# Optimization experiments

Hardware: AMD Instinct MI355X
Metric: run time of the kernel (lower is better)

## Reference

```python
import jax, jax.numpy as jnp
import numpy as np

LOSS_WEIGHT = 1.0
INTENSITY_WEIGHT = 0.5


def setup_inputs() -> dict:
    key = jax.random.key(0)
    k1, k2 = jax.random.split(key)
    N = 8192
    adv_pc = jax.random.normal(k1, (N, 4), dtype=jnp.float32)
    ori_pc = jax.random.normal(k2, (N, 4), dtype=jnp.float32)
    return {"adv_pc": adv_pc, "ori_pc": ori_pc}


def reference(adv_pc, ori_pc):
    # Scale the intensity channel (index 3) by intensity_weight, as in forward().
    scale = jnp.array([1.0, 1.0, 1.0, INTENSITY_WEIGHT], dtype=adv_pc.dtype)
    a = adv_pc * scale  # [N, 4]
    b = ori_pc * scale  # [M, 4]
    # knn_points with K=1 returns SQUARED euclidean distance to nearest neighbor.
    # Use the ||a||^2 + ||b||^2 - 2 a.b expansion to avoid an [N, M, 4] diff tensor.
    a2 = jnp.sum(a * a, axis=-1)          # [N]
    b2 = jnp.sum(b * b, axis=-1)          # [M]
    cross = jnp.einsum('nd,md->nm', a, b)  # [N, M]
    sqdist = a2[:, None] + b2[None, :] - 2.0 * cross  # [N, M]
    min_d = jnp.min(sqdist, axis=-1)      # per-adv-point nearest sq distance, [N]
    hd = jnp.max(min_d)                   # one-sided Hausdorff (squared)
    # original keeps the batch dim of size 1 after max(-1)
    return jnp.reshape(hd * LOSS_WEIGHT, (1,))
```

## Files before the change

kernel.cpp:

```cpp
#include <hip/hip_runtime.h>
#include <math.h>

#define THREADS 256
#define APT 4
#define TILE 64
#define RTHREADS 1024

__global__ __launch_bounds__(THREADS) void hd_min_atomic(
    const float* __restrict__ adv, const float* __restrict__ ori,
    int* __restrict__ mins,
    int N, int M, int chunks)
{
    __shared__ float4 sb[TILE];
    __shared__ __align__(16) float sb2[TILE];

    const int tid = threadIdx.x;
    const int base_i = blockIdx.x * (THREADS * APT) + tid;

    float4 a[APT];
    #pragma unroll
    for (int k = 0; k < APT; ++k) {
        int i = base_i + k * THREADS;
        float4 v = make_float4(0.f, 0.f, 0.f, 0.f);
        if (i < N) v = ((const float4*)adv)[i];
        a[k].x = -2.0f * v.x;
        a[k].y = -2.0f * v.y;
        a[k].z = -2.0f * v.z;
        a[k].w = -v.w;
    }

    float m[APT];
    #pragma unroll
    for (int k = 0; k < APT; ++k) m[k] = INFINITY;

    for (int base = blockIdx.y * TILE; base < M; base += chunks * TILE) {
        for (int k = tid; k < TILE; k += THREADS) {
            int j = base + k;
            float4 b = make_float4(0.f, 0.f, 0.f, 0.f);
            float b2 = INFINITY;
            if (j < M) {
                b = ((const float4*)ori)[j];
                b.w *= 0.5f;
                b2 = b.x*b.x + b.y*b.y + b.z*b.z + b.w*b.w;
            }
            sb[k]  = b;
            sb2[k] = b2;
        }
        __syncthreads();

        #pragma unroll 4
        for (int j = 0; j < TILE; j += 4) {
            float4 p0 = sb[j+0], p1 = sb[j+1], p2 = sb[j+2], p3 = sb[j+3];
            float4 q  = ((const float4*)sb2)[j >> 2];
            #pragma unroll
            for (int k = 0; k < APT; ++k) {
                float ax = a[k].x, ay = a[k].y, az = a[k].z, aw = a[k].w;
                float d0 = fmaf(ax, p0.x, fmaf(ay, p0.y, fmaf(az, p0.z, fmaf(aw, p0.w, q.x))));
                float d1 = fmaf(ax, p1.x, fmaf(ay, p1.y, fmaf(az, p1.z, fmaf(aw, p1.w, q.y))));
                float d2 = fmaf(ax, p2.x, fmaf(ay, p2.y, fmaf(az, p2.z, fmaf(aw, p2.w, q.z))));
                float d3 = fmaf(ax, p3.x, fmaf(ay, p3.y, fmaf(az, p3.z, fmaf(aw, p3.w, q.w))));
                m[k] = fminf(m[k], fminf(fminf(d0, d1), fminf(d2, d3)));
            }
        }
        __syncthreads();
    }

    #pragma unroll
    for (int k = 0; k < APT; ++k) {
        int i = base_i + k * THREADS;
        if (i < N) {
            float aa = a[k].x*a[k].x + a[k].y*a[k].y + a[k].z*a[k].z + a[k].w*a[k].w;
            float d  = fmaxf(fmaf(0.25f, aa, m[k]), 0.0f);
            atomicMin(&mins[i], __float_as_int(d));
        }
    }
}

__global__ __launch_bounds__(RTHREADS) void hd_final_max(
    const int* __restrict__ mins, float* __restrict__ out, int N)
{
    float m = 0.0f;
    for (int i = threadIdx.x; i < N; i += RTHREADS)
        m = fmaxf(m, __int_as_float(mins[i]));
    for (int off = 32; off >= 1; off >>= 1)
        m = fmaxf(m, __shfl_down(m, off, 64));
    __shared__ float smax[RTHREADS / 64];
    int lane = threadIdx.x & 63, wave = threadIdx.x >> 6;
    if (lane == 0) smax[wave] = m;
    __syncthreads();
    if (threadIdx.x == 0) {
        float bm = smax[0];
        #pragma unroll
        for (int w = 1; w < RTHREADS / 64; ++w) bm = fmaxf(bm, smax[w]);
        out[0] = bm;
    }
}

extern "C" void kernel_launch(void* const* d_in, const int* in_sizes, int n_in,
                              void* d_out, int out_size, void* d_ws, size_t ws_size,
                              hipStream_t stream) {
    const float* adv = (const float*)d_in[0];
    const float* ori = (const float*)d_in[1];
    float* out = (float*)d_out;
    int*   mins = (int*)d_ws;

    int N = in_sizes[0] / 4;
    int M = in_sizes[1] / 4;

    int gx    = (N + THREADS * APT - 1) / (THREADS * APT);
    int N_pad = gx * THREADS * APT;

    int maxtiles = (M + TILE - 1) / TILE;
    int chunks = 512 / gx;
    if (chunks < 1) chunks = 1;
    if (chunks > maxtiles) chunks = maxtiles;

    hipMemsetAsync(mins, 0x7F, (size_t)N_pad * sizeof(int), stream);

    hd_min_atomic<<<dim3(gx, chunks), THREADS, 0, stream>>>(
        adv, ori, mins, N, M, chunks);
    hd_final_max<<<1, RTHREADS, 0, stream>>>(mins, out, N);
}
```

Baseline: 68.10 us.

## Fuse nearest-neighbor min and Hausdorff max into one packed-FMA kernel

Replaces the memset, the atomicMin kernel and the final max kernel with a single kernel. Each block holds 16 adv points in registers as packed 2-wide vectors and streams all ori points straight from global memory. It reduces each point's minimum with wave shuffles and shared memory, then issues one atomicMax per block into the output. This removes two launches and the per-point workspace traffic, and the packed float2 FMAs aim to double ALU throughput. The trade-off is that every block re-reads the whole ori array (mostly from cache). The output is never zeroed before the atomicMax, so correctness depends on the initial contents of the output buffer.

```diff
diff --git a/kernel.cpp b/kernel.cpp
--- a/kernel.cpp
+++ b/kernel.cpp
@@ -2,97 +2,129 @@
 #include <math.h>
 
 #define THREADS 256
-#define APT 4
-#define TILE 64
-#define RTHREADS 1024
+#define APB 16
 
-__global__ __launch_bounds__(THREADS) void hd_min_atomic(
+typedef float v2f __attribute__((ext_vector_type(2)));
+
+__global__ __launch_bounds__(THREADS) void hd_onepass(
     const float* __restrict__ adv, const float* __restrict__ ori,
-    int* __restrict__ mins,
-    int N, int M, int chunks)
+    float* __restrict__ out, int N, int M)
 {
-    __shared__ float4 sb[TILE];
-    __shared__ __align__(16) float sb2[TILE];
+    __shared__ __align__(16) float4 sadv[APB];
+    __shared__ float sred[4][APB];
 
-    const int tid = threadIdx.x;
-    const int base_i = blockIdx.x * (THREADS * APT) + tid;
+    const int tid  = threadIdx.x;
+    const int base = blockIdx.x * APB;
 
-    float4 a[APT];
-    #pragma unroll
-    for (int k = 0; k < APT; ++k) {
-        int i = base_i + k * THREADS;
+    if (tid < APB) {
+        int i = base + tid;
         float4 v = make_float4(0.f, 0.f, 0.f, 0.f);
         if (i < N) v = ((const float4*)adv)[i];
-        a[k].x = -2.0f * v.x;
-        a[k].y = -2.0f * v.y;
-        a[k].z = -2.0f * v.z;
-        a[k].w = -v.w;
+        sadv[tid] = make_float4(-2.0f*v.x, -2.0f*v.y, -2.0f*v.z, -v.w);
+    }
+    __syncthreads();
+
+    v2f ax[APB/2], ay[APB/2], az[APB/2], aw[APB/2];
+    #pragma unroll
+    for (int p = 0; p < APB/2; ++p) {
+        float4 a0 = sadv[2*p], a1 = sadv[2*p + 1];
+        ax[p] = {a0.x, a1.x};
+        ay[p] = {a0.y, a1.y};
+        az[p] = {a0.z, a1.z};
+        aw[p] = {a0.w, a1.w};
     }
 
-    float m[APT];
+    float m[APB];
     #pragma unroll
-    for (int k = 0; k < APT; ++k) m[k] = INFINITY;
+    for (int k = 0; k < APB; ++k) m[k] = INFINITY;
 
-    for (int base = blockIdx.y * TILE; base < M; base += chunks * TILE) {
-        for (int k = tid; k < TILE; k += THREADS) {
-            int j = base + k;
-            float4 b = make_float4(0.f, 0.f, 0.f, 0.f);
-            float b2 = INFINITY;
-            if (j < M) {
-                b = ((const float4*)ori)[j];
-                b.w *= 0.5f;
-                b2 = b.x*b.x + b.y*b.y + b.z*b.z + b.w*b.w;
-            }
-            sb[k]  = b;
-            sb2[k] = b2;
+    const int NT = (M + THREADS - 1) / THREADS;
+
+    int t = 0;
+    #pragma unroll 2
+    for (; t + 1 < NT; t += 2) {
+        int j0 = t * THREADS + tid, j1 = j0 + THREADS;
+        float4 b0 = make_float4(0.f,0.f,0.f,0.f);
+        float4 b1 = make_float4(0.f,0.f,0.f,0.f);
+        float b20 = INFINITY, b21 = INFINITY;
+        if (j0 < M) {
+            b0 = ((const float4*)ori)[j0]; b0.w *= 0.5f;
+            b20 = b0.x*b0.x + b0.y*b0.y + b0.z*b0.z + b0.w*b0.w;
         }
-        __syncthreads();
-
-        #pragma unroll 4
-        for (int j = 0; j < TILE; j += 4) {
-            float4 p0 = sb[j+0], p1 = sb[j+1], p2 = sb[j+2], p3 = sb[j+3];
-            float4 q  = ((const float4*)sb2)[j >> 2];
-            #pragma unroll
-            for (int k = 0; k < APT; ++k) {
-                float ax = a[k].x, ay = a[k].y, az = a[k].z, aw = a[k].w;
-                float d0 = fmaf(ax, p0.x, fmaf(ay, p0.y, fmaf(az, p0.z, fmaf(aw, p0.w, q.x))));
-                float d1 = fmaf(ax, p1.x, fmaf(ay, p1.y, fmaf(az, p1.z, fmaf(aw, p1.w, q.y))));
-                float d2 = fmaf(ax, p2.x, fmaf(ay, p2.y, fmaf(az, p2.z, fmaf(aw, p2.w, q.z))));
-                float d3 = fmaf(ax, p3.x, fmaf(ay, p3.y, fmaf(az, p3.z, fmaf(aw, p3.w, q.w))));
-                m[k] = fminf(m[k], fminf(fminf(d0, d1), fminf(d2, d3)));
-            }
+        if (j1 < M) {
+            b1 = ((const float4*)ori)[j1]; b1.w *= 0.5f;
+            b21 = b1.x*b1.x + b1.y*b1.y + b1.z*b1.z + b1.w*b1.w;
         }
-        __syncthreads();
+        v2f bx0 = {b0.x, b0.x}, by0 = {b0.y, b0.y}, bz0 = {b0.z, b0.z}, bw0 = {b0.w, b0.w};
+        v2f bx1 = {b1.x, b1.x}, by1 = {b1.y, b1.y}, bz1 = {b1.z, b1.z}, bw1 = {b1.w, b1.w};
+        v2f q0  = {b20, b20},   q1  = {b21, b21};
+        #pragma unroll
+        for (int p = 0; p < APB/2; ++p) {
+            v2f t0 = q0;
+            t0 = aw[p] * bw0 + t0;
+            t0 = az[p] * bz0 + t0;
+            t0 = ay[p] * by0 + t0;
+            t0 = ax[p] * bx0 + t0;
+            v2f t1 = q1;
+            t1 = aw[p] * bw1 + t1;
+            t1 = az[p] * bz1 + t1;
+            t1 = ay[p] * by1 + t1;
+            t1 = ax[p] * bx1 + t1;
+            m[2*p]   = fminf(fminf(t0.x, t1.x), m[2*p]);
+            m[2*p+1] = fminf(fminf(t0.y, t1.y), m[2*p+1]);
+        }
+    }
+    for (; t < NT; ++t) {
+        int j0 = t * THREADS + tid;
+        float4 b0 = make_float4(0.f,0.f,0.f,0.f);
+        float b20 = INFINITY;
+        if (j0 < M) {
+            b0 = ((const float4*)ori)[j0]; b0.w *= 0.5f;
+            b20 = b0.x*b0.x + b0.y*b0.y + b0.z*b0.z + b0.w*b0.w;
+        }
+        v2f bx0 = {b0.x, b0.x}, by0 = {b0.y, b0.y}, bz0 = {b0.z, b0.z}, bw0 = {b0.w, b0.w};
+        v2f q0  = {b20, b20};
+        #pragma unroll
+        for (int p = 0; p < APB/2; ++p) {
+            v2f t0 = q0;
+            t0 = aw[p] * bw0 + t0;
+            t0 = az[p] * bz0 + t0;
+            t0 = ay[p] * by0 + t0;
+            t0 = ax[p] * bx0 + t0;
+            m[2*p]   = fminf(t0.x, m[2*p]);
+            m[2*p+1] = fminf(t0.y, m[2*p+1]);
+        }
     }
 
     #pragma unroll
-    for (int k = 0; k < APT; ++k) {
-        int i = base_i + k * THREADS;
-        if (i < N) {
-            float aa = a[k].x*a[k].x + a[k].y*a[k].y + a[k].z*a[k].z + a[k].w*a[k].w;
-            float d  = fmaxf(fmaf(0.25f, aa, m[k]), 0.0f);
-            atomicMin(&mins[i], __float_as_int(d));
+    for (int k = 0; k < APB; ++k) {
+        float v = m[k];
+        #pragma unroll
+        for (int off = 32; off >= 1; off >>= 1)
+            v = fminf(v, __shfl_xor(v, off, 64));
+        m[k] = v;
+    }
+    int lane = tid & 63, wave = tid >> 6;
+    if (lane == 0) {
+        #pragma unroll
+        for (int k = 0; k < APB; ++k) sred[wave][k] = m[k];
+    }
+    __syncthreads();
+
+    if (tid < 64) {
+        float d = 0.0f;
+        if (tid < APB && base + tid < N) {
+            float mm = fminf(fminf(sred[0][tid], sred[1][tid]),
+                             fminf(sred[2][tid], sred[3][tid]));
+            float4 a = sadv[tid];
+            float aa = a.x*a.x + a.y*a.y + a.z*a.z + a.w*a.w;
+            d = fmaxf(fmaf(0.25f, aa, mm), 0.0f);
         }
-    }
-}
-
-__global__ __launch_bounds__(RTHREADS) void hd_final_max(
-    const int* __restrict__ mins, float* __restrict__ out, int N)
-{
-    float m = 0.0f;
-    for (int i = threadIdx.x; i < N; i += RTHREADS)
-        m = fmaxf(m, __int_as_float(mins[i]));
-    for (int off = 32; off >= 1; off >>= 1)
-        m = fmaxf(m, __shfl_down(m, off, 64));
-    __shared__ float smax[RTHREADS / 64];
-    int lane = threadIdx.x & 63, wave = threadIdx.x >> 6;
-    if (lane == 0) smax[wave] = m;
-    __syncthreads();
-    if (threadIdx.x == 0) {
-        float bm = smax[0];
         #pragma unroll
-        for (int w = 1; w < RTHREADS / 64; ++w) bm = fmaxf(bm, smax[w]);
-        out[0] = bm;
+        for (int off = 32; off >= 1; off >>= 1)
+            d = fmaxf(d, __shfl_xor(d, off, 64));
+        if (tid == 0)
+            atomicMax((int*)out, __float_as_int(d));
     }
 }
 
@@ -102,22 +134,10 @@
     const float* adv = (const float*)d_in[0];
     const float* ori = (const float*)d_in[1];
     float* out = (float*)d_out;
-    int*   mins = (int*)d_ws;
 
     int N = in_sizes[0] / 4;
     int M = in_sizes[1] / 4;
 
-    int gx    = (N + THREADS * APT - 1) / (THREADS * APT);
-    int N_pad = gx * THREADS * APT;
-
-    int maxtiles = (M + TILE - 1) / TILE;
-    int chunks = 512 / gx;
-    if (chunks < 1) chunks = 1;
-    if (chunks > maxtiles) chunks = maxtiles;
-
-    hipMemsetAsync(mins, 0x7F, (size_t)N_pad * sizeof(int), stream);
-
-    hd_min_atomic<<<dim3(gx, chunks), THREADS, 0, stream>>>(
-        adv, ori, mins, N, M, chunks);
-    hd_final_max<<<1, RTHREADS, 0, stream>>>(mins, out, N);
+    int blocks = (N + APB - 1) / APB;
+    hd_onepass<<<blocks, THREADS, 0, stream>>>(adv, ori, out, N, M);
 }
```

Result: slower. 73.65 us (+8.2%).
